# Performance work log

Hardware: AMD Instinct MI355X
Metric: run time of the kernel (lower is better)

## Reference

```python
import jax, jax.numpy as jnp
import numpy as np

SAMPLE_RATE = 16000
SOUND_SPEED = 343.0
MAX_ORDER = 15
RIR_LENGTH = 3968
WINDOW_LENGTH = 81
PAD = WINDOW_LENGTH // 2  # 40

# Static image-source lattice (depends only on max_order): all integer
# reflection index triplets with |nx|+|ny|+|nz| <= max_order.
_ind = np.arange(-MAX_ORDER, MAX_ORDER + 1)
_grid = np.stack(np.meshgrid(_ind, _ind, _ind, indexing="ij"), -1).reshape(-1, 3)
XYZ = _grid[np.abs(_grid).sum(1) <= MAX_ORDER].astype(np.float32)  # (I,3), I=4991
EXP_LO = np.abs(np.floor(XYZ / 2)).astype(np.float32)        # hits on lower walls per dim
EXP_HI = np.abs(np.floor((XYZ + 1) / 2)).astype(np.float32)  # hits on upper walls per dim


def _hann(x, T):
    # continuous Hann window sampled at non-integer points, zero outside |x|<=T/2
    return jnp.where(jnp.abs(x) <= T / 2, 0.5 * (1.0 + jnp.cos(2.0 * jnp.pi * x / T)), 0.0)


def _forward(inp):
    room = inp[:, 0:3]                 # (B,3) room dimensions [m]
    mic = inp[:, 3:6] * room           # (B,3)
    src = inp[:, 6:9] * room           # (B,3)
    a_w = inp[:, 9:10]
    absorption = jnp.concatenate([a_w, a_w, a_w, a_w, inp[:, 10:11], inp[:, 11:12]], axis=1)
    absorption = absorption * 0.84 + 0.01            # (B,6): [x-,x+,y-,y+,floor,ceiling]
    tr = jnp.sqrt(1.0 - absorption)                  # wall reflection coefficients

    xyz = jnp.asarray(XYZ)                           # (I,3)
    d = room[:, None, :]
    s = src[:, None, :]
    # image source locations (B,I,3): mirror parity per torchaudio ISM
    img_loc = jnp.where(xyz % 2 == 1, d * (xyz + 1.0) - s, d * xyz + s)
    # per-image-source attenuation (B,I)
    t_lo = tr[:, None, 0::2]                         # (B,1,3) lower walls per dim
    t_hi = tr[:, None, 1::2]                         # (B,1,3) upper walls per dim
    att = jnp.prod(t_lo ** jnp.asarray(EXP_LO) * t_hi ** jnp.asarray(EXP_HI), axis=-1)

    dist = jnp.linalg.norm(img_loc - mic[:, None, :], axis=-1)   # (B,I)
    amp = att / dist                                              # 1/r spreading
    delay = dist * (SAMPLE_RATE / SOUND_SPEED)                    # fractional sample delay
    delay_i = jnp.ceil(delay)

    # windowed-sinc fractional-delay pulse sampled at n = delay_i-PAD .. delay_i+PAD
    n_rel = jnp.arange(-PAD, PAD + 1, dtype=jnp.float32)          # (W,)
    x = delay_i[..., None] + n_rel - delay[..., None]             # (B,I,W)
    sig = amp[..., None] * jnp.sinc(x) * _hann(x, 2 * PAD)        # (B,I,W)

    # scatter-accumulate pulses at time index n, dropping out-of-range samples
    t_idx = (delay_i[..., None] + n_rel).astype(jnp.int32)        # (B,I,W)
    B = inp.shape[0]
    b_idx = jnp.arange(B, dtype=jnp.int32)[:, None, None]
    rir = jnp.zeros((B, RIR_LENGTH), dtype=sig.dtype).at[b_idx, t_idx].add(sig, mode="drop")

    toa = PAD + SAMPLE_RATE * jnp.linalg.norm(mic - src, axis=1) / SOUND_SPEED  # (B,)
    return rir, toa


def setup_inputs():
    key = jax.random.key(0)
    u = jax.random.uniform(key, (128, 12), dtype=jnp.float32)
    room = 2.0 + 8.0 * u[:, :3]          # room dims in [2,10] m
    rest = 0.05 + 0.9 * u[:, 3:]         # mic/src fractions and absorptions in (0,1)
    return {"input": jnp.concatenate([room, rest], axis=1)}


def reference(input):
    return _forward(input)
```

## Files before the change

kernel.cpp:

```cpp
#include <hip/hip_runtime.h>

#define NIMG    4991
#define RIRLEN  3968
#define NT      512
#define NGRP    4
#define KPT     10
#define INV_PI  0.31830988618379067f
#define SR_OVER_C 46.647230320699704f

struct Tab { int v[NIMG]; };
static constexpr Tab make_tab() {
    Tab t{};
    int k = 0;
    for (int x = -15; x <= 15; ++x)
        for (int y = -15; y <= 15; ++y)
            for (int z = -15; z <= 15; ++z) {
                int ax = x < 0 ? -x : x;
                int ay = y < 0 ? -y : y;
                int az = z < 0 ? -z : z;
                if (ax + ay + az <= 15)
                    t.v[k++] = (x + 15) | ((y + 15) << 8) | ((z + 15) << 16);
            }
    return t;
}
__constant__ Tab c_tab = make_tab();

static __device__ __forceinline__ int iabs(int v) { return v < 0 ? -v : v; }

typedef __fp16 f16x2 __attribute__((ext_vector_type(2)));

__global__ __launch_bounds__(NT, 4)
void rir_fused(const float* __restrict__ inp, float* __restrict__ out, int B) {
    const int bx   = blockIdx.x;
    const int b    = bx >> 2;
    const int g    = bx & 3;
    const int tid  = threadIdx.x;
    const int lane = tid & 63;
    const int wv   = tid >> 6;
    const int q    = lane & 3;

    __shared__ float2   s_dh[NIMG];
    __shared__ unsigned s_cs[NIMG];
    __shared__ float    s_par[12];
    __shared__ int      s_h4[256][4];
    __shared__ int      s_off[257];

    for (int k = tid; k < 1024; k += NT) ((int*)s_h4)[k] = 0;
    if (tid == 0) {
        const float* ip = inp + b * 12;
        float rx = ip[0], ry = ip[1], rz = ip[2];
        float mx = ip[3] * rx, my = ip[4] * ry, mz = ip[5] * rz;
        float sx = ip[6] * rx, sy = ip[7] * ry, sz = ip[8] * rz;
        float aw = __builtin_fmaf(ip[9],  0.84f, 0.01f);
        float a4 = __builtin_fmaf(ip[10], 0.84f, 0.01f);
        float a5 = __builtin_fmaf(ip[11], 0.84f, 0.01f);
        s_par[0] = rx; s_par[1] = ry; s_par[2] = rz;
        s_par[3] = mx; s_par[4] = my; s_par[5] = mz;
        s_par[6] = sx; s_par[7] = sy; s_par[8] = sz;
        s_par[9]  = 0.5f * __builtin_amdgcn_logf(1.0f - aw);
        s_par[10] = 0.5f * __builtin_amdgcn_logf(1.0f - a4);
        s_par[11] = 0.5f * __builtin_amdgcn_logf(1.0f - a5);
        if (g == 0) {
            float dx = mx - sx, dy = my - sy, dz = mz - sz;
            out[(size_t)B * RIRLEN + b] = __builtin_fmaf(
                __builtin_sqrtf(dx * dx + dy * dy + dz * dz), SR_OVER_C, 40.0f);
        }
    }
    __syncthreads();

    const float rx = s_par[0], ry = s_par[1], rz = s_par[2];
    const float mx = s_par[3], my = s_par[4], mz = s_par[5];
    const float sx = s_par[6], sy = s_par[7], sz = s_par[8];
    const float lw = s_par[9], l4 = s_par[10], l5 = s_par[11];
    const int   fb = 4 * g + 1;

    float2   edh[KPT];
    unsigned ecs[KPT];
    int      bkt[KPT];
    #pragma unroll
    for (int k = 0; k < KPT; ++k) {
        bkt[k] = -1;
        const int idx = tid + k * NT;
        if (idx < NIMG) {
            const int p = c_tab.v[idx];
            const int x = (p & 255) - 15;
            const int y = ((p >> 8) & 255) - 15;
            const int z = ((p >> 16) & 255) - 15;
            const float ix = (x & 1) ? __builtin_fmaf(rx, (float)(x + 1), -sx)
                                     : __builtin_fmaf(rx, (float)x, sx);
            const float iy = (y & 1) ? __builtin_fmaf(ry, (float)(y + 1), -sy)
                                     : __builtin_fmaf(ry, (float)y, sy);
            const float iz = (z & 1) ? __builtin_fmaf(rz, (float)(z + 1), -sz)
                                     : __builtin_fmaf(rz, (float)z, sz);
            const float dx = ix - mx, dy = iy - my, dz = iz - mz;
            const float dist  = __builtin_sqrtf(
                __builtin_fmaf(dx, dx, __builtin_fmaf(dy, dy, dz * dz)));
            const float delay = dist * SR_OVER_C;
            const float di    = __builtin_ceilf(delay);
            const int   ti0   = (int)di - 40;
            const int   bk    = (ti0 + 96) >> 4;
            const bool owned  = ((unsigned)((bk - fb + 16) & 15) < 9u);
            if (ti0 < RIRLEN && owned) {
                const int ew = iabs(x >> 1) + iabs((x + 1) >> 1)
                             + iabs(y >> 1) + iabs((y + 1) >> 1);
                const float att = __builtin_amdgcn_exp2f(__builtin_fmaf((float)ew, lw,
                                      __builtin_fmaf((float)iabs(z >> 1), l4,
                                           (float)iabs((z + 1) >> 1) * l5)));
                const float amp = att * __builtin_amdgcn_rcpf(dist);
                float frac = di - delay;
                if (frac == 0.0f) frac = di * 1.52587890625e-05f;
                const int dii = (int)di;
                float c1p = amp * __builtin_amdgcn_sinf(0.5f * frac) * INV_PI;
                if (dii & 1) c1p = -c1p;
                const float Hp     = 0.5f * c1p;
                const float dstore = di - frac;
                const float rv = dstore * 0.0125f;
                const float fr = rv - __builtin_floorf(rv);
                const float Hcd = Hp * __builtin_amdgcn_cosf(fr);
                const float Hsd = Hp * __builtin_amdgcn_sinf(fr);
                const f16x2 pk2 = __builtin_amdgcn_cvt_pkrtz(Hcd, Hsd);

                bkt[k] = bk;
                edh[k] = make_float2(dstore, Hp);
                ecs[k] = __builtin_bit_cast(unsigned, pk2);
                atomicAdd(&s_h4[bk][q], 1);
            }
        }
    }
    __syncthreads();

    if (wv == 0) {
        const int l = lane;
        const int4 a0 = *(const int4*)&s_h4[4 * l + 0][0];
        const int4 a1 = *(const int4*)&s_h4[4 * l + 1][0];
        const int4 a2 = *(const int4*)&s_h4[4 * l + 2][0];
        const int4 a3 = *(const int4*)&s_h4[4 * l + 3][0];
        const int c0 = a0.x + a0.y + a0.z + a0.w;
        const int c1 = a1.x + a1.y + a1.z + a1.w;
        const int c2 = a2.x + a2.y + a2.z + a2.w;
        const int c3 = a3.x + a3.y + a3.z + a3.w;
        const int ts = c0 + c1 + c2 + c3;
        int incl = ts;
        #pragma unroll
        for (int d = 1; d < 64; d <<= 1) {
            const int u = __shfl_up(incl, d, 64);
            if (l >= d) incl += u;
        }
        const int base = incl - ts;
        s_off[4 * l + 0] = base;
        s_off[4 * l + 1] = base + c0;
        s_off[4 * l + 2] = base + c0 + c1;
        s_off[4 * l + 3] = base + c0 + c1 + c2;
        if (l == 63) s_off[256] = incl;
    }
    __syncthreads();

    if (tid < 256) {
        int run = s_off[tid];
        #pragma unroll
        for (int p = 0; p < 4; ++p) {
            const int c = s_h4[tid][p];
            s_h4[tid][p] = run;
            run += c;
        }
    }
    __syncthreads();

    #pragma unroll
    for (int k = 0; k < KPT; ++k) {
        if (bkt[k] >= 0) {
            const int slot = atomicAdd(&s_h4[bkt[k]][q], 1);
            s_dh[slot] = edh[k];
            s_cs[slot] = ecs[k];
        }
    }
    __syncthreads();

    int T = 0;
    #pragma unroll
    for (int kk = 0; kk < 16; ++kk) {
        const int wi = g + 4 * kk;
        if (wi < 62) T += s_off[4 * wi + 10] - s_off[4 * wi + 1];
    }

    int P = 0;
    #pragma unroll
    for (int kk = 0; kk < 16; ++kk) {
        const int wi = g + 4 * kk;
        if (wi >= 62) break;
        const int lo  = s_off[4 * wi + 1];
        const int hi  = s_off[4 * wi + 10];
        const int len = hi - lo;
        int owner = (T > 0)
            ? (int)((8u * (unsigned)(P + (len >> 1))) / (unsigned)T)
            : (kk >> 1);
        if (owner > 7) owner = 7;
        P += len;
        if (owner != wv) continue;

        const int   t    = (wi << 6) + lane;
        const float tf   = (float)t;
        const int   m    = t - (t / 80) * 80;
        const float cth0 = __builtin_amdgcn_cosf((float)m * 0.0125f);
        const float sth0 = __builtin_amdgcn_sinf((float)m * 0.0125f);
        const float sl   = (lane & 1) ? -1.0f : 1.0f;

        float acc = 0.0f;
        #pragma unroll 4
        for (int i = lo; i < hi; ++i) {
            const float2 e  = s_dh[i];
            const f16x2  h  = __builtin_bit_cast(f16x2, s_cs[i]);
            const float xw  = tf - e.x;
            const float pre = __builtin_fmaf(cth0, (float)h.x,
                                  __builtin_fmaf(sth0, (float)h.y, e.y));
            const float hm  = (__builtin_fabsf(xw) <= 40.0f) ? pre : 0.0f;
            acc = __builtin_fmaf(hm, __builtin_amdgcn_rcpf(xw), acc);
        }
        out[(size_t)b * RIRLEN + t] = sl * acc;
    }
}

extern "C" void kernel_launch(void* const* d_in, const int* in_sizes, int n_in,
                              void* d_out, int out_size, void* d_ws, size_t ws_size,
                              hipStream_t stream) {
    (void)d_ws; (void)ws_size; (void)n_in; (void)out_size;
    const float* inp = (const float*)d_in[0];
    float* out = (float*)d_out;
    const int B = in_sizes[0] / 12;
    rir_fused<<<dim3(B * NGRP), dim3(NT), 0, stream>>>(inp, out, B);
}
```

Measured before the change: 103.1 us.

## Split each batch across eight blocks and balance window work across waves at element granularity

Doubles the number of blocks per batch item (8 groups, each owning every 8th 64-sample window), so each block scatters and evaluates fewer pulses. Work inside a block is now split evenly by pulse count across the 8 waves, with partial window sums combined through shared-memory float atomics, replacing whole-window assignment to waves. The second-pass atomics are dropped by recording each pulse's rank during the histogram pass. The inner loop reads two pulses at a time with vectorized shared loads. In exchange, each block still recomputes all 4991 image sources, so that per-block overhead is now paid twice as often, and the final sums go through an extra synchronisation and shared-memory atomics.

```diff
diff --git a/kernel.cpp b/kernel.cpp
--- a/kernel.cpp
+++ b/kernel.cpp
@@ -3,7 +3,7 @@
 #define NIMG    4991
 #define RIRLEN  3968
 #define NT      512
-#define NGRP    4
+#define NGRP    8
 #define KPT     10
 #define INV_PI  0.31830988618379067f
 #define SR_OVER_C 46.647230320699704f
@@ -32,20 +32,22 @@
 __global__ __launch_bounds__(NT, 4)
 void rir_fused(const float* __restrict__ inp, float* __restrict__ out, int B) {
     const int bx   = blockIdx.x;
-    const int b    = bx >> 2;
-    const int g    = bx & 3;
+    const int b    = bx >> 3;
+    const int g    = bx & 7;
     const int tid  = threadIdx.x;
     const int lane = tid & 63;
     const int wv   = tid >> 6;
     const int q    = lane & 3;
 
-    __shared__ float2   s_dh[NIMG];
-    __shared__ unsigned s_cs[NIMG];
+    __shared__ __align__(16) float2   s_dh[NIMG];
+    __shared__ __align__(8)  unsigned s_cs[NIMG];
     __shared__ float    s_par[12];
     __shared__ int      s_h4[256][4];
     __shared__ int      s_off[257];
+    __shared__ float    s_acc[8][64];
 
     for (int k = tid; k < 1024; k += NT) ((int*)s_h4)[k] = 0;
+    if (tid < 512) ((float*)s_acc)[tid] = 0.0f;
     if (tid == 0) {
         const float* ip = inp + b * 12;
         float rx = ip[0], ry = ip[1], rz = ip[2];
@@ -72,14 +74,14 @@
     const float mx = s_par[3], my = s_par[4], mz = s_par[5];
     const float sx = s_par[6], sy = s_par[7], sz = s_par[8];
     const float lw = s_par[9], l4 = s_par[10], l5 = s_par[11];
-    const int   fb = 4 * g + 1;
+    const int   fb = (4 * g + 1) & 31;
 
     float2   edh[KPT];
     unsigned ecs[KPT];
-    int      bkt[KPT];
+    int      enc[KPT];
     #pragma unroll
     for (int k = 0; k < KPT; ++k) {
-        bkt[k] = -1;
+        enc[k] = -1;
         const int idx = tid + k * NT;
         if (idx < NIMG) {
             const int p = c_tab.v[idx];
@@ -99,7 +101,7 @@
             const float di    = __builtin_ceilf(delay);
             const int   ti0   = (int)di - 40;
             const int   bk    = (ti0 + 96) >> 4;
-            const bool owned  = ((unsigned)((bk - fb + 16) & 15) < 9u);
+            const bool owned  = ((unsigned)((bk - fb + 32) & 31) < 9u);
             if (ti0 < RIRLEN && owned) {
                 const int ew = iabs(x >> 1) + iabs((x + 1) >> 1)
                              + iabs(y >> 1) + iabs((y + 1) >> 1);
@@ -120,10 +122,10 @@
                 const float Hsd = Hp * __builtin_amdgcn_sinf(fr);
                 const f16x2 pk2 = __builtin_amdgcn_cvt_pkrtz(Hcd, Hsd);
 
-                bkt[k] = bk;
+                const int rnk = atomicAdd(&s_h4[bk][q], 1);
+                enc[k] = (bk << 13) | rnk;
                 edh[k] = make_float2(dstore, Hp);
                 ecs[k] = __builtin_bit_cast(unsigned, pk2);
-                atomicAdd(&s_h4[bk][q], 1);
             }
         }
     }
@@ -168,55 +170,79 @@
 
     #pragma unroll
     for (int k = 0; k < KPT; ++k) {
-        if (bkt[k] >= 0) {
-            const int slot = atomicAdd(&s_h4[bkt[k]][q], 1);
+        if (enc[k] >= 0) {
+            const int bk   = enc[k] >> 13;
+            const int slot = s_h4[bk][q] + (enc[k] & 8191);
             s_dh[slot] = edh[k];
             s_cs[slot] = ecs[k];
         }
     }
     __syncthreads();
 
-    int T = 0;
-    #pragma unroll
-    for (int kk = 0; kk < 16; ++kk) {
-        const int wi = g + 4 * kk;
-        if (wi < 62) T += s_off[4 * wi + 10] - s_off[4 * wi + 1];
-    }
-
-    int P = 0;
-    #pragma unroll
-    for (int kk = 0; kk < 16; ++kk) {
-        const int wi = g + 4 * kk;
-        if (wi >= 62) break;
-        const int lo  = s_off[4 * wi + 1];
-        const int hi  = s_off[4 * wi + 10];
-        const int len = hi - lo;
-        int owner = (T > 0)
-            ? (int)((8u * (unsigned)(P + (len >> 1))) / (unsigned)T)
-            : (kk >> 1);
-        if (owner > 7) owner = 7;
-        P += len;
-        if (owner != wv) continue;
-
+    int wlo[8], wlen[8], wpre[8];
+    int T = 0, nw = 0;
+    #pragma unroll
+    for (int kk = 0; kk < 8; ++kk) {
+        const int wi = g + 8 * kk;
+        wpre[kk] = T;
+        if (wi < 62) {
+            wlo[kk]  = s_off[4 * wi + 1];
+            wlen[kk] = s_off[4 * wi + 10] - wlo[kk];
+            T += wlen[kk];
+            nw = kk + 1;
+        } else { wlo[kk] = 0; wlen[kk] = 0; }
+    }
+    const int a0r = (T * wv) >> 3;
+    const int a1r = (T * (wv + 1)) >> 3;
+
+#define EV1(DLY, HPV, PKU) do {                                              \
+        const f16x2 hh = __builtin_bit_cast(f16x2, (PKU));                   \
+        const float xw = tf - (DLY);                                         \
+        const float pre = __builtin_fmaf(cth0, (float)hh.x,                  \
+                              __builtin_fmaf(sth0, (float)hh.y, (HPV)));     \
+        const float hm = (__builtin_fabsf(xw) <= 40.0f) ? pre : 0.0f;        \
+        acc = __builtin_fmaf(hm, __builtin_amdgcn_rcpf(xw), acc);            \
+    } while (0)
+
+    #pragma unroll
+    for (int kk = 0; kk < 8; ++kk) {
+        if (wlen[kk] == 0) continue;
+        const int o0 = (wpre[kk] > a0r) ? wpre[kk] : a0r;
+        const int oe = ((wpre[kk] + wlen[kk]) < a1r) ? (wpre[kk] + wlen[kk]) : a1r;
+        if (o0 >= oe) continue;
+        int       i  = wlo[kk] + (o0 - wpre[kk]);
+        const int ie = wlo[kk] + (oe - wpre[kk]);
+
+        const int   wi   = g + 8 * kk;
         const int   t    = (wi << 6) + lane;
         const float tf   = (float)t;
         const int   m    = t - (t / 80) * 80;
         const float cth0 = __builtin_amdgcn_cosf((float)m * 0.0125f);
         const float sth0 = __builtin_amdgcn_sinf((float)m * 0.0125f);
-        const float sl   = (lane & 1) ? -1.0f : 1.0f;
 
         float acc = 0.0f;
-        #pragma unroll 4
-        for (int i = lo; i < hi; ++i) {
-            const float2 e  = s_dh[i];
-            const f16x2  h  = __builtin_bit_cast(f16x2, s_cs[i]);
-            const float xw  = tf - e.x;
-            const float pre = __builtin_fmaf(cth0, (float)h.x,
-                                  __builtin_fmaf(sth0, (float)h.y, e.y));
-            const float hm  = (__builtin_fabsf(xw) <= 40.0f) ? pre : 0.0f;
-            acc = __builtin_fmaf(hm, __builtin_amdgcn_rcpf(xw), acc);
-        }
-        out[(size_t)b * RIRLEN + t] = sl * acc;
+        if ((i < ie) && (i & 1)) {
+            EV1(s_dh[i].x, s_dh[i].y, s_cs[i]); ++i;
+        }
+        for (; i + 2 <= ie; i += 2) {
+            const float4 dd = *(const float4*)&s_dh[i];
+            const uint2  cc = *(const uint2*)&s_cs[i];
+            EV1(dd.x, dd.y, cc.x);
+            EV1(dd.z, dd.w, cc.y);
+        }
+        if (i < ie) EV1(s_dh[i].x, s_dh[i].y, s_cs[i]);
+
+        atomicAdd(&s_acc[kk][lane], acc);
+    }
+#undef EV1
+    __syncthreads();
+
+    if (tid < 64 * nw) {
+        const int kk = tid >> 6;
+        const int wi = g + 8 * kk;
+        const int t  = (wi << 6) + lane;
+        const float sl = (lane & 1) ? -1.0f : 1.0f;
+        out[(size_t)b * RIRLEN + t] = sl * s_acc[kk][lane];
     }
 }
 
```

Measured after the change: 100.0 us. -3.0%, faster.
